# Optimization experiments

Hardware: AMD Instinct MI355X
Metric: run time of the kernel (lower is better)

Reference implementation:

```python
import jax, jax.numpy as jnp
import numpy as np

HID = 2048        # hidden_size
STATE = 128       # ssm state size N
HEADS = 64
HEADDIM = 64
GROUPS = 1
K = 4             # conv kernel
INTER = 4096      # expand * hidden_size == HEADS * HEADDIM
CONV_DIM = INTER + 2 * GROUPS * STATE   # 4352
PROJ = INTER + CONV_DIM + HEADS         # 8512
EPS = 1e-5


def setup_inputs() -> dict:
    ks = jax.random.split(jax.random.key(0), 8)
    hidden_states = jax.random.normal(ks[0], (2, 2048, HID), dtype=jnp.float32)
    norm_weight = jnp.ones((HID,), jnp.float32)
    in_proj_w = jax.random.normal(ks[1], (PROJ, HID), jnp.float32) * 0.02
    conv_w = jax.random.normal(ks[2], (CONV_DIM, 1, K), jnp.float32) * 0.1
    conv_b = jax.random.normal(ks[3], (CONV_DIM,), jnp.float32) * 0.02
    dt_bias = jax.random.normal(ks[4], (HEADS,), jnp.float32) * 0.5
    A_log = jnp.log(jnp.arange(1, HEADS + 1, dtype=jnp.float32))
    D = jnp.ones((HEADS,), jnp.float32)
    gate_norm_weight = jnp.ones((INTER,), jnp.float32)
    out_proj_w = jax.random.normal(ks[5], (HID, INTER), jnp.float32) * 0.02
    return {"hidden_states": hidden_states, "norm_weight": norm_weight,
            "in_proj_w": in_proj_w, "conv_w": conv_w, "conv_b": conv_b,
            "dt_bias": dt_bias, "A_log": A_log, "D": D,
            "gate_norm_weight": gate_norm_weight, "out_proj_w": out_proj_w}


def _rmsnorm(x, w, eps):
    v = jnp.mean(jnp.square(x.astype(jnp.float32)), axis=-1, keepdims=True)
    return (x * jax.lax.rsqrt(v + eps)) * w


def _mamba2_block(hidden_states, norm_weight, in_proj_w, conv_w, conv_b,
                  dt_bias, A_log, D, gate_norm_weight, out_proj_w):
    b, s, _ = hidden_states.shape
    residual = hidden_states.astype(jnp.float32)  # residual_in_fp32
    x = _rmsnorm(hidden_states, norm_weight, EPS)

    proj = x @ in_proj_w.T                                  # [b,s,PROJ]
    gate, xBC, dt = jnp.split(proj, [INTER, INTER + CONV_DIM], axis=-1)

    # causal depthwise conv1d over channels, then SiLU
    xBC_t = jnp.swapaxes(xBC, 1, 2)                          # [b,C,s]
    conv = jax.lax.conv_general_dilated(
        xBC_t, conv_w, window_strides=(1,), padding=[(K - 1, 0)],
        dimension_numbers=("NCH", "OIH", "NCH"), feature_group_count=CONV_DIM)
    xBC = jax.nn.silu(jnp.swapaxes(conv + conv_b[None, :, None], 1, 2))

    xs, B, C = jnp.split(xBC, [INTER, INTER + GROUPS * STATE], axis=-1)
    hg = HEADS // GROUPS
    xs = xs.reshape(b, s, GROUPS, hg, HEADDIM)
    B = B.reshape(b, s, GROUPS, STATE)
    C = C.reshape(b, s, GROUPS, STATE)

    dt = jax.nn.softplus(dt + dt_bias).reshape(b, s, GROUPS, hg)  # [b,s,g,hg]
    A = -jnp.exp(A_log).reshape(GROUPS, hg)
    dA = jnp.exp(dt * A)                                     # [b,s,g,hg]
    dtx = dt[..., None] * xs                                  # [b,s,g,hg,p]

    def step(state, inp):
        dA_t, dtx_t, B_t, C_t = inp
        # state: [b,g,hg,p,n]
        state = state * dA_t[..., None, None] + jnp.einsum("bghp,bgn->bghpn", dtx_t, B_t)
        y_t = jnp.einsum("bghpn,bgn->bghp", state, C_t)
        return state, y_t

    mv = lambda a: jnp.moveaxis(a, 1, 0)  # time-major for scan
    state0 = jnp.zeros((b, GROUPS, hg, HEADDIM, STATE), jnp.float32)
    _, y = jax.lax.scan(step, state0, (mv(dA), mv(dtx), mv(B), mv(C)))
    y = jnp.moveaxis(y, 0, 1)                                 # [b,s,g,hg,p]
    y = y + D.reshape(GROUPS, hg)[..., None] * xs             # skip term
    y = y.reshape(b, s, INTER)

    # gated RMSNorm then output projection
    y = _rmsnorm(y * jax.nn.silu(gate), gate_norm_weight, EPS)
    out = y @ out_proj_w.T
    return residual + out


def reference(hidden_states, norm_weight, in_proj_w, conv_w, conv_b,
              dt_bias, A_log, D, gate_norm_weight, out_proj_w):
    return _mamba2_block(hidden_states, norm_weight, in_proj_w, conv_w, conv_b,
                         dt_bias, A_log, D, gate_norm_weight, out_proj_w)
```

## Files before the change

### kernel.cpp

```cpp
#include <hip/hip_runtime.h>
#include <math.h>

#define HID      2048
#define STATE    128
#define HEADS    64
#define HEADDIM  64
#define INTER    4096
#define CONV_DIM 4352
#define PROJ     8512
#define NBATCH   2
#define SEQ      2048
#define BS       (NBATCH*SEQ)
#define EPS      1e-5f
#define YN_COL   4160

typedef __attribute__((ext_vector_type(8))) short short8;
typedef __attribute__((ext_vector_type(4))) float f32x4;

__device__ inline unsigned short f2bf(float f) {
  union { float f; unsigned int u; } v; v.f = f;
  unsigned int r = v.u + 0x7fffu + ((v.u >> 16) & 1u);
  return (unsigned short)(r >> 16);
}
__device__ inline float bf2f(unsigned short b) {
  union { unsigned int u; float f; } v; v.u = ((unsigned int)b) << 16;
  return v.f;
}

__global__ __launch_bounds__(256)
void cast_bf16_kernel(const float4* __restrict__ src, ushort4* __restrict__ dst, int n4) {
  int i = blockIdx.x * 256 + threadIdx.x;
  if (i >= n4) return;
  float4 v = src[i];
  ushort4 o;
  o.x = f2bf(v.x); o.y = f2bf(v.y); o.z = f2bf(v.z); o.w = f2bf(v.w);
  dst[i] = o;
}

__global__ __launch_bounds__(256)
void rmsnorm_in_kernel(const float* __restrict__ x, const float* __restrict__ w,
                       unsigned short* __restrict__ xn) {
  int row = blockIdx.x;
  int t = threadIdx.x;
  const float* xr = x + (size_t)row * HID;
  float4 a = ((const float4*)xr)[t];
  float4 b = ((const float4*)xr)[t + 256];
  float ss = a.x*a.x + a.y*a.y + a.z*a.z + a.w*a.w
           + b.x*b.x + b.y*b.y + b.z*b.z + b.w*b.w;
  for (int o = 32; o > 0; o >>= 1) ss += __shfl_down(ss, o);
  __shared__ float red[4];
  __shared__ float scl;
  if ((t & 63) == 0) red[t >> 6] = ss;
  __syncthreads();
  if (t == 0) scl = rsqrtf((red[0]+red[1]+red[2]+red[3]) / (float)HID + EPS);
  __syncthreads();
  float s = scl;
  float4 w0 = ((const float4*)w)[t];
  float4 w1 = ((const float4*)w)[t + 256];
  ushort4 o0, o1;
  o0.x = f2bf(a.x*s*w0.x); o0.y = f2bf(a.y*s*w0.y); o0.z = f2bf(a.z*s*w0.z); o0.w = f2bf(a.w*s*w0.w);
  o1.x = f2bf(b.x*s*w1.x); o1.y = f2bf(b.y*s*w1.y); o1.z = f2bf(b.z*s*w1.z); o1.w = f2bf(b.w*s*w1.w);
  ushort4* dst = (ushort4*)(xn + (size_t)row * HID);
  dst[t] = o0;
  dst[t + 256] = o1;
}


__device__ __forceinline__ void stage_half64(const unsigned short* __restrict__ G, int ld,
                                             int row0, int rmax, int kt,
                                             unsigned short* lbase, int half, int t) {
  const int w = t >> 6;
#pragma unroll
  for (int it = 0; it < 2; ++it) {
    int id = it * 256 + t;
    int rl = id >> 3;
    int sl = id & 7;
    int grow = row0 + half * 64 + rl;
    if (grow > rmax) grow = rmax;
    const unsigned short* g = G + (size_t)grow * ld + kt * 64 + ((sl ^ (rl & 7)) << 3);
    unsigned short* l = lbase + half * (64 * 64) + (it * 256 + w * 64) * 8;
    __builtin_amdgcn_global_load_lds((const __attribute__((address_space(1))) void*)g,
                                     (__attribute__((address_space(3))) void*)l, 16, 0, 0);
  }
}

#define VMW4 asm volatile("s_waitcnt vmcnt(4)" ::: "memory")

#define PHASE(BUF, MH, NH, RA, RB, STG, VMW_)                                        \
  {                                                                                  \
    const unsigned short* bufA = lds + (BUF)*16384;                                  \
    const unsigned short* bufB = lds + (BUF)*16384 + 8192;                           \
    if (RA) {                                                                        \
      _Pragma("unroll")                                                              \
      for (int ml = 0; ml < 2; ++ml) {                                               \
        _Pragma("unroll")                                                            \
        for (int kk = 0; kk < 2; ++kk) {                                             \
          const int r = wr*64 + (MH)*32 + ml*16 + tq;                                \
          aR[ml][kk] = *(const short8*)(bufA + r*64 + (((kk<<2)|quad)^(r&7))*8);     \
        }                                                                            \
      }                                                                              \
    }                                                                                \
    if (RB) {                                                                        \
      _Pragma("unroll")                                                              \
      for (int nl = 0; nl < 2; ++nl) {                                               \
        _Pragma("unroll")                                                            \
        for (int kk = 0; kk < 2; ++kk) {                                             \
          const int r = wc*64 + (NH)*32 + nl*16 + tq;                                \
          bR[NH][nl][kk] = *(const short8*)(bufB + r*64 + (((kk<<2)|quad)^(r&7))*8); \
        }                                                                            \
      }                                                                              \
    }                                                                                \
    STG;                                                                             \
    __builtin_amdgcn_s_barrier();                                                    \
    asm volatile("s_waitcnt lgkmcnt(0)" ::: "memory");                               \
    __builtin_amdgcn_sched_barrier(0);                                               \
    __builtin_amdgcn_s_setprio(1);                                                   \
    _Pragma("unroll")                                                                \
    for (int ml = 0; ml < 2; ++ml) {                                                 \
      _Pragma("unroll")                                                              \
      for (int nl = 0; nl < 2; ++nl) {                                               \
        _Pragma("unroll")                                                            \
        for (int kk = 0; kk < 2; ++kk) {                                             \
          acc[(MH)*2+ml][(NH)*2+nl] = __builtin_amdgcn_mfma_f32_16x16x32_bf16(       \
              aR[ml][kk], bR[NH][nl][kk], acc[(MH)*2+ml][(NH)*2+nl], 0, 0, 0);       \
        }                                                                            \
      }                                                                              \
    }                                                                                \
    __builtin_amdgcn_s_setprio(0);                                                   \
    VMW_;                                                                            \
    __builtin_amdgcn_s_barrier();                                                    \
  }

__global__ __launch_bounds__(256, 2)
void gemm128_kernel(const unsigned short* __restrict__ A, int lda,
                    const unsigned short* __restrict__ B,
                    float* __restrict__ Cf, unsigned short* __restrict__ Cb, int ldc,
                    int M, int N, int Kd, const float* __restrict__ residual) {
  __shared__ unsigned short lds[32768];
  const int t = threadIdx.x;
  const int lane = t & 63;
  const int quad = lane >> 4;
  const int tq = lane & 15;
  const int w = t >> 6;
  const int wr = w >> 1;
  const int wc = w & 1;

  const int Mtiles = M >> 7;
  const int Ntiles = (N + 127) >> 7;
  const int nwg = (int)gridDim.x;
  const int cpx = nwg >> 3;
  const int bid = (int)blockIdx.x;
  const int sw = (bid & 7) * cpx + (bid >> 3);
  const int NBfull = Ntiles & ~7;
  int m0, n0;
  if (sw < Mtiles * NBfull) {
    int brick = sw >> 6;
    int inner = sw & 63;
    int bm = brick % (Mtiles >> 3);
    int bn = brick / (Mtiles >> 3);
    m0 = (bm * 8 + (inner & 7)) << 7;
    n0 = (bn * 8 + (inner >> 3)) << 7;
  } else {
    int r = sw - Mtiles * NBfull;
    m0 = (r % Mtiles) << 7;
    n0 = (NBfull + r / Mtiles) << 7;
  }

  f32x4 acc[4][4];
#pragma unroll
  for (int i = 0; i < 4; ++i)
#pragma unroll
    for (int j = 0; j < 4; ++j) acc[i][j] = (f32x4){0.f, 0.f, 0.f, 0.f};

  short8 aR[2][2];
  short8 bR[2][2][2];

  unsigned short* A0 = lds;
  unsigned short* B0 = lds + 8192;
  unsigned short* A1 = lds + 16384;
  unsigned short* B1 = lds + 24576;

  const int kIters = Kd >> 6;
  const int nIter  = kIters >> 1;

  stage_half64(A, lda, m0, M - 1, 0, A0, 0, t);
  stage_half64(A, lda, m0, M - 1, 0, A0, 1, t);
  stage_half64(B, Kd,  n0, N - 1, 0, B0, 0, t);
  stage_half64(B, Kd,  n0, N - 1, 0, B0, 1, t);
  stage_half64(B, Kd,  n0, N - 1, 1, B1, 0, t);
  stage_half64(B, Kd,  n0, N - 1, 1, B1, 1, t);
  VMW4;
  __builtin_amdgcn_s_barrier();

  for (int i = 0; i < nIter; ++i) {
    const int k1 = 2 * i + 1;
    int k2 = 2 * i + 2; if (k2 > kIters - 1) k2 = kIters - 1;
    int k3 = 2 * i + 3; if (k3 > kIters - 1) k3 = kIters - 1;
    PHASE(0, 0, 0, 1, 1, stage_half64(A, lda, m0, M - 1, k1, A1, 0, t), ((void)0))
    PHASE(0, 0, 1, 0, 1, stage_half64(A, lda, m0, M - 1, k1, A1, 1, t), ((void)0))
    PHASE(0, 1, 1, 1, 0, stage_half64(B, Kd,  n0, N - 1, k2, B0, 0, t), ((void)0))
    PHASE(0, 1, 0, 0, 0, stage_half64(B, Kd,  n0, N - 1, k2, B0, 1, t), VMW4)
    PHASE(1, 0, 0, 1, 1, stage_half64(A, lda, m0, M - 1, k2, A0, 0, t), ((void)0))
    PHASE(1, 0, 1, 0, 1, stage_half64(A, lda, m0, M - 1, k2, A0, 1, t), ((void)0))
    PHASE(1, 1, 1, 1, 0, stage_half64(B, Kd,  n0, N - 1, k3, B1, 0, t), ((void)0))
    PHASE(1, 1, 0, 0, 0, stage_half64(B, Kd,  n0, N - 1, k3, B1, 1, t), VMW4)
  }
  asm volatile("s_waitcnt vmcnt(0)" ::: "memory");

#pragma unroll
  for (int mf = 0; mf < 4; ++mf) {
    const int rowb = m0 + wr * 64 + mf * 16 + quad * 4;
#pragma unroll
    for (int nf = 0; nf < 4; ++nf) {
      const int col = n0 + wc * 64 + nf * 16 + tq;
      if (col < N) {
        if (Cb) {
#pragma unroll
          for (int r = 0; r < 4; ++r)
            Cb[(size_t)(rowb + r) * ldc + col] = f2bf(acc[mf][nf][r]);
        } else {
#pragma unroll
          for (int r = 0; r < 4; ++r) {
            size_t idx = (size_t)(rowb + r) * N + col;
            float v = acc[mf][nf][r];
            if (residual) v += residual[idx];
            Cf[idx] = v;
          }
        }
      }
    }
  }
}

#define CONV_BC 128
#define CONV_BS 64
#define CXS 136

__global__ __launch_bounds__(256)
void conv_dt_kernel(const unsigned short* __restrict__ proj, const float* __restrict__ cw,
                    const float* __restrict__ cb, const float* __restrict__ dtb,
                    const float* __restrict__ A_log,
                    unsigned short* __restrict__ convo, float2* __restrict__ dts) {
  const int NCB = CONV_DIM / CONV_BC;
  const int NCONVB = NCB * (BS / CONV_BS);
  int blk = blockIdx.x;
  int t = threadIdx.x;
  if (blk < NCONVB) {
    __shared__ unsigned short xs[67 * CXS];
    int cblk = blk % NCB;
    int rblk = blk / NCB;
    int ch0 = cblk * CONV_BC;
    int rs0 = rblk * CONV_BS;
    int s0 = rs0 & (SEQ - 1);
    const int c8 = t & 15;
    const int co = c8 * 8;
    float cwr[4][8], cbr[8];
#pragma unroll
    for (int e = 0; e < 8; e++) {
      cbr[e] = cb[ch0 + co + e];
#pragma unroll
      for (int k = 0; k < 4; k++) cwr[k][e] = cw[(ch0 + co + e) * 4 + k];
    }
    for (int i = t; i < 67 * 16; i += 256) {
      int row = i >> 4, sl = i & 15;
      short8 v;
      if (s0 == 0 && row < 3) v = (short8){0,0,0,0,0,0,0,0};
      else v = *(const short8*)&proj[(size_t)(rs0 - 3 + row) * PROJ + INTER + ch0 + sl * 8];
      *(short8*)&xs[row * CXS + sl * 8] = v;
    }
    __syncthreads();
#pragma unroll
    for (int it = 0; it < 4; ++it) {
      int r = (t >> 4) + it * 16;
      float acc[8];
#pragma unroll
      for (int e = 0; e < 8; e++) acc[e] = cbr[e];
#pragma unroll
      for (int k = 0; k < 4; k++) {
        short8 v = *(const short8*)&xs[(r + k) * CXS + co];
#pragma unroll
        for (int e = 0; e < 8; e++) acc[e] += bf2f((unsigned short)v[e]) * cwr[k][e];
      }
      short8 o;
#pragma unroll
      for (int e = 0; e < 8; e++) {
        float a = acc[e];
        o[e] = (short)f2bf(a * __builtin_amdgcn_rcpf(1.f + __expf(-a)));
      }
      *(short8*)&convo[(size_t)(rs0 + r) * CONV_DIM + ch0 + co] = o;
    }
  } else {
    int k = (blk - NCONVB) * 256 + t;
    if (k < BS * HEADS) {
      int h  = k & 63;
      int rs = k >> 6;
      float x = bf2f(proj[(size_t)rs * PROJ + INTER + CONV_DIM + h]) + dtb[h];
      float dt = (x > 20.f) ? x : log1pf(__expf(x));
      float Ah = -__expf(A_log[h]);
      dts[k] = make_float2(dt, dt * Ah);
    }
  }
}

#define LCH 64
#define SR  128
#define BR  64
#define TST 72
#define SWZ(r,c) ((((c) ^ ((r) & 7)) << 3))
#define LBAR do { asm volatile("s_waitcnt lgkmcnt(0)" ::: "memory"); \
                  __builtin_amdgcn_s_barrier(); } while (0)

__global__ __launch_bounds__(512)
void ssd_scan_kernel(const unsigned short* __restrict__ convo, const float2* __restrict__ dts,
                     unsigned short* __restrict__ yp) {
  __shared__ unsigned short Cst[64 * SR];
  __shared__ unsigned short Bst[64 * SR];
  __shared__ unsigned short Btt[128 * BR];
  __shared__ unsigned short xtT[32 * TST];
  __shared__ unsigned short Msh[64 * TST];
  __shared__ unsigned short Sb[2][32 * SR];
  __shared__ float dtaL[64], dtvL[64];

  const int ph = blockIdx.x & 1;
  const int h  = (blockIdx.x >> 1) & 63;
  const int b  = blockIdx.x >> 7;
  const int t  = threadIdx.x;
  const int wv = t >> 6;
  const int lane = t & 63;
  const int quad = lane >> 4;
  const int tq   = lane & 15;
  const size_t row0 = (size_t)b * SEQ;
  const int xcol = h * 64 + ph * 32;

  for (int i = t; i < 32 * SR; i += 512) Sb[0][i] = 0;

  f32x4 s_acc[4];
#pragma unroll
  for (int c = 0; c < 4; c++) s_acc[c] = (f32x4){0.f, 0.f, 0.f, 0.f};
  const int pt  = wv & 1;
  const int ntb = ((wv >> 1) & 1) * 4;

  short8 vb_r[2], vc_r[2]; ushort4 vx_r; float2 dv_r = make_float2(0.f, 0.f);
  {
#pragma unroll
    for (int it = 0; it < 2; ++it) {
      int id = t + 512 * it;
      int row = id >> 4, cc = id & 15;
      size_t g = (row0 + row) * CONV_DIM + INTER;
      vb_r[it] = *(const short8*)&convo[g + cc * 8];
      vc_r[it] = *(const short8*)&convo[g + STATE + cc * 8];
    }
    int row = t >> 3, c = t & 7;
    vx_r = *(const ushort4*)&convo[(row0 + row) * CONV_DIM + xcol + c * 4];
    if (t < 64) dv_r = dts[((row0 + t) << 6) + h];
  }

  int pp = 0;
  for (int c0 = 0; c0 < SEQ; c0 += LCH, pp ^= 1) {
    LBAR;
#pragma unroll
    for (int it = 0; it < 2; ++it) {
      int id = t + 512 * it;
      int row = id >> 4, cc = id & 15;
      *(short8*)&Bst[row * SR + SWZ(row, cc)] = vb_r[it];
      *(short8*)&Cst[row * SR + SWZ(row, cc)] = vc_r[it];
    }
    {
      int row = t >> 3, c = t & 7;
      xtT[(c * 4 + 0) * TST + row] = vx_r.x;
      xtT[(c * 4 + 1) * TST + row] = vx_r.y;
      xtT[(c * 4 + 2) * TST + row] = vx_r.z;
      xtT[(c * 4 + 3) * TST + row] = vx_r.w;
    }
    if (t < 64) { dtvL[t] = dv_r.x; dtaL[t] = dv_r.y; }
    LBAR;

#pragma unroll
    for (int bi = 0; bi < 2; ++bi) {
      int q = t + 512 * bi;
      int n = q & 127, jc = q >> 7;
      short8 o;
#pragma unroll
      for (int s = 0; s < 8; ++s)
        o[s] = (short)Bst[(jc * 8 + s) * SR + SWZ(jc * 8 + s, n >> 3) + (n & 7)];
      *(short8*)&Btt[n * BR + SWZ(n, jc)] = o;
    }

    float v = dtaL[lane];
#pragma unroll
    for (int off = 1; off < 64; off <<= 1) {
      float u = __shfl_up(v, off);
      if (lane >= off) v += u;
    }
    float tot = __shfl(v, 63);

    LBAR;

    if (c0 + LCH < SEQ) {
#pragma unroll
      for (int it = 0; it < 2; ++it) {
        int id = t + 512 * it;
        int row = id >> 4, cc = id & 15;
        size_t g = (row0 + c0 + LCH + row) * CONV_DIM + INTER;
        vb_r[it] = *(const short8*)&convo[g + cc * 8];
        vc_r[it] = *(const short8*)&convo[g + STATE + cc * 8];
      }
      int row = t >> 3, c = t & 7;
      vx_r = *(const ushort4*)&convo[(row0 + c0 + LCH + row) * CONV_DIM + xcol + c * 4];
      if (t < 64) dv_r = dts[((row0 + c0 + LCH + t) << 6) + h];
    }

    if (wv < 4) {
      short8 afC[4];
#pragma unroll
      for (int kt = 0; kt < 4; kt++)
        afC[kt] = *(const short8*)&Cst[(16 * wv + tq) * SR + SWZ(16 * wv + tq, kt * 4 + quad)];
      f32x4 g_acc[4];
#pragma unroll
      for (int nj = 0; nj < 4; nj++) g_acc[nj] = (f32x4){0.f, 0.f, 0.f, 0.f};
#pragma unroll
      for (int kt = 0; kt < 4; kt++) {
#pragma unroll
        for (int nj = 0; nj < 4; nj++) {
          short8 bfr = *(const short8*)&Bst[(16 * nj + tq) * SR + SWZ(16 * nj + tq, kt * 4 + quad)];
          g_acc[nj] = __builtin_amdgcn_mfma_f32_16x16x32_bf16(afC[kt], bfr, g_acc[nj], 0, 0, 0);
        }
      }
      float ci[4], pex[4];
#pragma unroll
      for (int r = 0; r < 4; r++) {
        ci[r] = __shfl(v, 16 * wv + quad * 4 + r);
        pex[r] = __expf(ci[r]);
      }
#pragma unroll
      for (int nj = 0; nj < 4; nj++) {
        int j = 16 * nj + tq;
        float cj = __shfl(v, j);
        float dj = dtvL[j];
#pragma unroll
        for (int r = 0; r < 4; r++) {
          int i = 16 * wv + quad * 4 + r;
          float val = (j <= i) ? g_acc[nj][r] * __expf(ci[r] - cj) * dj : 0.f;
          Msh[i * TST + j] = f2bf(val);
        }
      }
      f32x4 yac[2];
      yac[0] = (f32x4){0.f, 0.f, 0.f, 0.f};
      yac[1] = (f32x4){0.f, 0.f, 0.f, 0.f};
#pragma unroll
      for (int kt = 0; kt < 4; kt++) {
#pragma unroll
        for (int np = 0; np < 2; np++) {
          short8 bs = *(const short8*)&Sb[pp][(16 * np + tq) * SR + SWZ(16 * np + tq, kt * 4 + quad)];
          yac[np] = __builtin_amdgcn_mfma_f32_16x16x32_bf16(afC[kt], bs, yac[np], 0, 0, 0);
        }
      }
#pragma unroll
      for (int np = 0; np < 2; np++)
#pragma unroll
        for (int r = 0; r < 4; r++) yac[np][r] *= pex[r];
#pragma unroll
      for (int kt2 = 0; kt2 < 2; kt2++) {
        short8 am = *(const short8*)&Msh[(16 * wv + tq) * TST + kt2 * 32 + quad * 8];
#pragma unroll
        for (int np = 0; np < 2; np++) {
          short8 bx = *(const short8*)&xtT[(16 * np + tq) * TST + kt2 * 32 + quad * 8];
          yac[np] = __builtin_amdgcn_mfma_f32_16x16x32_bf16(am, bx, yac[np], 0, 0, 0);
        }
      }
#pragma unroll
      for (int np = 0; np < 2; np++) {
#pragma unroll
        for (int r = 0; r < 4; r++) {
          int i = 16 * wv + quad * 4 + r;
          int p = ph * 32 + 16 * np + tq;
          yp[(row0 + c0 + i) * INTER + h * 64 + p] = f2bf(yac[np][r]);
        }
      }
    } else {
      float ptot = __expf(tot);
      short8 ax[2];
#pragma unroll
      for (int kt2 = 0; kt2 < 2; kt2++) {
        short8 xv = *(const short8*)&xtT[(16 * pt + tq) * TST + kt2 * 32 + quad * 8];
#pragma unroll
        for (int e = 0; e < 8; e++) {
          int j = kt2 * 32 + quad * 8 + e;
          float cj = __shfl(v, j);
          float wj = __expf(tot - cj) * dtvL[j];
          ax[kt2][e] = (short)f2bf(bf2f((unsigned short)xv[e]) * wj);
        }
      }
#pragma unroll
      for (int c = 0; c < 4; c++)
#pragma unroll
        for (int r = 0; r < 4; r++) s_acc[c][r] *= ptot;
#pragma unroll
      for (int kt2 = 0; kt2 < 2; kt2++) {
#pragma unroll
        for (int c = 0; c < 4; c++) {
          short8 bb = *(const short8*)&Btt[(16 * (ntb + c) + tq) * BR + SWZ(16 * (ntb + c) + tq, kt2 * 4 + quad)];
          s_acc[c] = __builtin_amdgcn_mfma_f32_16x16x32_bf16(ax[kt2], bb, s_acc[c], 0, 0, 0);
        }
      }
#pragma unroll
      for (int c = 0; c < 4; c++)
#pragma unroll
        for (int r = 0; r < 4; r++) {
          int p = 16 * pt + quad * 4 + r;
          int n = 16 * (ntb + c) + tq;
          Sb[pp ^ 1][p * SR + SWZ(p, n >> 3) + (n & 7)] = f2bf(s_acc[c][r]);
        }
    }
  }
}

__global__ __launch_bounds__(256)
void gated_norm_kernel(const unsigned short* __restrict__ yp,
                       const unsigned short* __restrict__ convo, const unsigned short* __restrict__ proj,
                       const float* __restrict__ Dv, const float* __restrict__ gnw,
                       unsigned short* __restrict__ yn) {
  int row = blockIdx.x;
  int t = threadIdx.x;
  __shared__ float red[4];
  __shared__ float scl;
  size_t yo = (size_t)row * INTER;
  size_t co = (size_t)row * CONV_DIM;
  size_t po = (size_t)row * PROJ;
  float vv[16];
  float ss = 0.f;
#pragma unroll
  for (int c = 0; c < 4; c++) {
    int i = t * 4 + c * 1024;
    ushort4 y0 = *(const ushort4*)&yp[yo + i];
    ushort4 xs = *(const ushort4*)&convo[co + i];
    ushort4 g  = *(const ushort4*)&proj[po + i];
    float Dh = Dv[i >> 6];
    float yv[4] = { bf2f(y0.x) + Dh * bf2f(xs.x),
                    bf2f(y0.y) + Dh * bf2f(xs.y),
                    bf2f(y0.z) + Dh * bf2f(xs.z),
                    bf2f(y0.w) + Dh * bf2f(xs.w) };
    float gv[4] = { bf2f(g.x), bf2f(g.y), bf2f(g.z), bf2f(g.w) };
#pragma unroll
    for (int k = 0; k < 4; k++) {
      float val = yv[k] * (gv[k] * __builtin_amdgcn_rcpf(1.f + __expf(-gv[k])));
      vv[c * 4 + k] = val;
      ss += val * val;
    }
  }
  for (int o = 32; o > 0; o >>= 1) ss += __shfl_down(ss, o);
  if ((t & 63) == 0) red[t >> 6] = ss;
  __syncthreads();
  if (t == 0) scl = rsqrtf((red[0]+red[1]+red[2]+red[3]) / (float)INTER + EPS);
  __syncthreads();
  float s = scl;
#pragma unroll
  for (int c = 0; c < 4; c++) {
    int i = t * 4 + c * 1024;
    ushort4 o;
    o.x = f2bf(vv[c*4+0] * s * gnw[i + 0]);
    o.y = f2bf(vv[c*4+1] * s * gnw[i + 1]);
    o.z = f2bf(vv[c*4+2] * s * gnw[i + 2]);
    o.w = f2bf(vv[c*4+3] * s * gnw[i + 3]);
    *(ushort4*)&yn[po + i] = o;
  }
}

extern "C" void kernel_launch(void* const* d_in, const int* in_sizes, int n_in,
                              void* d_out, int out_size, void* d_ws, size_t ws_size,
                              hipStream_t stream) {
  const float* hidden  = (const float*)d_in[0];
  const float* norm_w  = (const float*)d_in[1];
  const float* w1      = (const float*)d_in[2];
  const float* convw   = (const float*)d_in[3];
  const float* convb   = (const float*)d_in[4];
  const float* dt_bias = (const float*)d_in[5];
  const float* A_log   = (const float*)d_in[6];
  const float* Dv      = (const float*)d_in[7];
  const float* gnw     = (const float*)d_in[8];
  const float* w2      = (const float*)d_in[9];
  float* out = (float*)d_out;

  char* ws = (char*)d_ws;
  size_t off = 0;
  auto alloc = [&](size_t bytes) {
    void* p = ws + off;
    off += (bytes + 255) & ~(size_t)255;
    return p;
  };
  unsigned short* XN  = (unsigned short*)alloc((size_t)BS * HID * 2);
  unsigned short* W1B = (unsigned short*)alloc((size_t)PROJ * HID * 2);
  unsigned short* W2B = (unsigned short*)alloc((size_t)HID * INTER * 2);
  unsigned short* PRJ = (unsigned short*)alloc((size_t)BS * PROJ * 2);
  unsigned short* CVO = (unsigned short*)alloc((size_t)BS * CONV_DIM * 2);
  float2*         DTS = (float2*)alloc((size_t)BS * HEADS * 8);
  unsigned short* YP  = XN;
  unsigned short* YN  = PRJ + YN_COL;
  if (off > ws_size) return;
  (void)in_sizes; (void)n_in; (void)out_size;

  int n1 = PROJ * HID / 4;
  cast_bf16_kernel<<<(n1 + 255) / 256, 256, 0, stream>>>((const float4*)w1, (ushort4*)W1B, n1);
  int n2 = HID * INTER / 4;
  cast_bf16_kernel<<<(n2 + 255) / 256, 256, 0, stream>>>((const float4*)w2, (ushort4*)W2B, n2);

  rmsnorm_in_kernel<<<BS, 256, 0, stream>>>(hidden, norm_w, XN);

  gemm128_kernel<<<dim3((BS / 128) * ((PROJ + 127) / 128)), 256, 0, stream>>>(
      XN, HID, W1B, nullptr, PRJ, PROJ, BS, PROJ, HID, nullptr);

  conv_dt_kernel<<<(CONV_DIM / CONV_BC) * (BS / CONV_BS) + (BS * HEADS) / 256, 256, 0, stream>>>(
      PRJ, convw, convb, dt_bias, A_log, CVO, DTS);

  ssd_scan_kernel<<<256, 512, 0, stream>>>(CVO, DTS, YP);

  gated_norm_kernel<<<BS, 256, 0, stream>>>(YP, CVO, PRJ, Dv, gnw, YN);

  gemm128_kernel<<<dim3((BS / 128) * (HID / 128)), 256, 0, stream>>>(
      YN, PROJ, W2B, out, nullptr, HID, BS, HID, INTER, hidden);
}
```

Before: 528.8 us.

## Make GEMM kernels persistent with atomic tile counter scheduling

Both GEMMs now launch a fixed grid of 512 workgroups that pull tiles from a global atomic counter until all tiles are done, instead of one workgroup per tile with a swizzled brick mapping. This aims to cut tail imbalance and launch overhead. The trade-off is a simple column-major tile order (m fastest) in place of the L2-friendly 8x8 brick swizzle, plus one atomic and extra barriers per tile. A memset resets the counters on every call.

```diff
diff --git a/kernel.cpp b/kernel.cpp
--- a/kernel.cpp
+++ b/kernel.cpp
@@ -135,8 +135,10 @@
 void gemm128_kernel(const unsigned short* __restrict__ A, int lda,
                     const unsigned short* __restrict__ B,
                     float* __restrict__ Cf, unsigned short* __restrict__ Cb, int ldc,
-                    int M, int N, int Kd, const float* __restrict__ residual) {
+                    int M, int N, int Kd, const float* __restrict__ residual,
+                    unsigned int* __restrict__ counter, int nTiles) {
   __shared__ unsigned short lds[32768];
+  __shared__ unsigned int sw_sh;
   const int t = threadIdx.x;
   const int lane = t & 63;
   const int quad = lane >> 4;
@@ -146,89 +148,79 @@
   const int wc = w & 1;
 
   const int Mtiles = M >> 7;
-  const int Ntiles = (N + 127) >> 7;
-  const int nwg = (int)gridDim.x;
-  const int cpx = nwg >> 3;
-  const int bid = (int)blockIdx.x;
-  const int sw = (bid & 7) * cpx + (bid >> 3);
-  const int NBfull = Ntiles & ~7;
-  int m0, n0;
-  if (sw < Mtiles * NBfull) {
-    int brick = sw >> 6;
-    int inner = sw & 63;
-    int bm = brick % (Mtiles >> 3);
-    int bn = brick / (Mtiles >> 3);
-    m0 = (bm * 8 + (inner & 7)) << 7;
-    n0 = (bn * 8 + (inner >> 3)) << 7;
-  } else {
-    int r = sw - Mtiles * NBfull;
-    m0 = (r % Mtiles) << 7;
-    n0 = (NBfull + r / Mtiles) << 7;
-  }
-
-  f32x4 acc[4][4];
-#pragma unroll
-  for (int i = 0; i < 4; ++i)
-#pragma unroll
-    for (int j = 0; j < 4; ++j) acc[i][j] = (f32x4){0.f, 0.f, 0.f, 0.f};
-
-  short8 aR[2][2];
-  short8 bR[2][2][2];
+  const int kIters = Kd >> 6;
+  const int nIter  = kIters >> 1;
 
   unsigned short* A0 = lds;
   unsigned short* B0 = lds + 8192;
   unsigned short* A1 = lds + 16384;
   unsigned short* B1 = lds + 24576;
 
-  const int kIters = Kd >> 6;
-  const int nIter  = kIters >> 1;
-
-  stage_half64(A, lda, m0, M - 1, 0, A0, 0, t);
-  stage_half64(A, lda, m0, M - 1, 0, A0, 1, t);
-  stage_half64(B, Kd,  n0, N - 1, 0, B0, 0, t);
-  stage_half64(B, Kd,  n0, N - 1, 0, B0, 1, t);
-  stage_half64(B, Kd,  n0, N - 1, 1, B1, 0, t);
-  stage_half64(B, Kd,  n0, N - 1, 1, B1, 1, t);
-  VMW4;
-  __builtin_amdgcn_s_barrier();
-
-  for (int i = 0; i < nIter; ++i) {
-    const int k1 = 2 * i + 1;
-    int k2 = 2 * i + 2; if (k2 > kIters - 1) k2 = kIters - 1;
-    int k3 = 2 * i + 3; if (k3 > kIters - 1) k3 = kIters - 1;
-    PHASE(0, 0, 0, 1, 1, stage_half64(A, lda, m0, M - 1, k1, A1, 0, t), ((void)0))
-    PHASE(0, 0, 1, 0, 1, stage_half64(A, lda, m0, M - 1, k1, A1, 1, t), ((void)0))
-    PHASE(0, 1, 1, 1, 0, stage_half64(B, Kd,  n0, N - 1, k2, B0, 0, t), ((void)0))
-    PHASE(0, 1, 0, 0, 0, stage_half64(B, Kd,  n0, N - 1, k2, B0, 1, t), VMW4)
-    PHASE(1, 0, 0, 1, 1, stage_half64(A, lda, m0, M - 1, k2, A0, 0, t), ((void)0))
-    PHASE(1, 0, 1, 0, 1, stage_half64(A, lda, m0, M - 1, k2, A0, 1, t), ((void)0))
-    PHASE(1, 1, 1, 1, 0, stage_half64(B, Kd,  n0, N - 1, k3, B1, 0, t), ((void)0))
-    PHASE(1, 1, 0, 0, 0, stage_half64(B, Kd,  n0, N - 1, k3, B1, 1, t), VMW4)
-  }
-  asm volatile("s_waitcnt vmcnt(0)" ::: "memory");
-
-#pragma unroll
-  for (int mf = 0; mf < 4; ++mf) {
-    const int rowb = m0 + wr * 64 + mf * 16 + quad * 4;
-#pragma unroll
-    for (int nf = 0; nf < 4; ++nf) {
-      const int col = n0 + wc * 64 + nf * 16 + tq;
-      if (col < N) {
-        if (Cb) {
-#pragma unroll
-          for (int r = 0; r < 4; ++r)
-            Cb[(size_t)(rowb + r) * ldc + col] = f2bf(acc[mf][nf][r]);
-        } else {
-#pragma unroll
-          for (int r = 0; r < 4; ++r) {
-            size_t idx = (size_t)(rowb + r) * N + col;
-            float v = acc[mf][nf][r];
-            if (residual) v += residual[idx];
-            Cf[idx] = v;
+  short8 aR[2][2];
+  short8 bR[2][2][2];
+
+  for (;;) {
+    if (t == 0) sw_sh = atomicAdd(counter, 1u);
+    __syncthreads();
+    const unsigned int sw = sw_sh;
+    if (sw >= (unsigned int)nTiles) break;
+    const int m0 = (int)(sw % (unsigned int)Mtiles) << 7;
+    const int n0 = (int)(sw / (unsigned int)Mtiles) << 7;
+
+    f32x4 acc[4][4];
+#pragma unroll
+    for (int i = 0; i < 4; ++i)
+#pragma unroll
+      for (int j = 0; j < 4; ++j) acc[i][j] = (f32x4){0.f, 0.f, 0.f, 0.f};
+
+    stage_half64(A, lda, m0, M - 1, 0, A0, 0, t);
+    stage_half64(A, lda, m0, M - 1, 0, A0, 1, t);
+    stage_half64(B, Kd,  n0, N - 1, 0, B0, 0, t);
+    stage_half64(B, Kd,  n0, N - 1, 0, B0, 1, t);
+    stage_half64(B, Kd,  n0, N - 1, 1, B1, 0, t);
+    stage_half64(B, Kd,  n0, N - 1, 1, B1, 1, t);
+    VMW4;
+    __builtin_amdgcn_s_barrier();
+
+    for (int i = 0; i < nIter; ++i) {
+      const int k1 = 2 * i + 1;
+      int k2 = 2 * i + 2; if (k2 > kIters - 1) k2 = kIters - 1;
+      int k3 = 2 * i + 3; if (k3 > kIters - 1) k3 = kIters - 1;
+      PHASE(0, 0, 0, 1, 1, stage_half64(A, lda, m0, M - 1, k1, A1, 0, t), ((void)0))
+      PHASE(0, 0, 1, 0, 1, stage_half64(A, lda, m0, M - 1, k1, A1, 1, t), ((void)0))
+      PHASE(0, 1, 1, 1, 0, stage_half64(B, Kd,  n0, N - 1, k2, B0, 0, t), ((void)0))
+      PHASE(0, 1, 0, 0, 0, stage_half64(B, Kd,  n0, N - 1, k2, B0, 1, t), VMW4)
+      PHASE(1, 0, 0, 1, 1, stage_half64(A, lda, m0, M - 1, k2, A0, 0, t), ((void)0))
+      PHASE(1, 0, 1, 0, 1, stage_half64(A, lda, m0, M - 1, k2, A0, 1, t), ((void)0))
+      PHASE(1, 1, 1, 1, 0, stage_half64(B, Kd,  n0, N - 1, k3, B1, 0, t), ((void)0))
+      PHASE(1, 1, 0, 0, 0, stage_half64(B, Kd,  n0, N - 1, k3, B1, 1, t), VMW4)
+    }
+    asm volatile("s_waitcnt vmcnt(0)" ::: "memory");
+
+#pragma unroll
+    for (int mf = 0; mf < 4; ++mf) {
+      const int rowb = m0 + wr * 64 + mf * 16 + quad * 4;
+#pragma unroll
+      for (int nf = 0; nf < 4; ++nf) {
+        const int col = n0 + wc * 64 + nf * 16 + tq;
+        if (col < N) {
+          if (Cb) {
+#pragma unroll
+            for (int r = 0; r < 4; ++r)
+              Cb[(size_t)(rowb + r) * ldc + col] = f2bf(acc[mf][nf][r]);
+          } else {
+#pragma unroll
+            for (int r = 0; r < 4; ++r) {
+              size_t idx = (size_t)(rowb + r) * N + col;
+              float v = acc[mf][nf][r];
+              if (residual) v += residual[idx];
+              Cf[idx] = v;
+            }
           }
         }
       }
     }
+    __syncthreads();
   }
 }
 
@@ -588,6 +580,7 @@
     off += (bytes + 255) & ~(size_t)255;
     return p;
   };
+  unsigned int*   CTR = (unsigned int*)alloc(256);
   unsigned short* XN  = (unsigned short*)alloc((size_t)BS * HID * 2);
   unsigned short* W1B = (unsigned short*)alloc((size_t)PROJ * HID * 2);
   unsigned short* W2B = (unsigned short*)alloc((size_t)HID * INTER * 2);
@@ -599,6 +592,8 @@
   if (off > ws_size) return;
   (void)in_sizes; (void)n_in; (void)out_size;
 
+  hipMemsetAsync(CTR, 0, 256, stream);
+
   int n1 = PROJ * HID / 4;
   cast_bf16_kernel<<<(n1 + 255) / 256, 256, 0, stream>>>((const float4*)w1, (ushort4*)W1B, n1);
   int n2 = HID * INTER / 4;
@@ -606,8 +601,9 @@
 
   rmsnorm_in_kernel<<<BS, 256, 0, stream>>>(hidden, norm_w, XN);
 
-  gemm128_kernel<<<dim3((BS / 128) * ((PROJ + 127) / 128)), 256, 0, stream>>>(
-      XN, HID, W1B, nullptr, PRJ, PROJ, BS, PROJ, HID, nullptr);
+  gemm128_kernel<<<512, 256, 0, stream>>>(
+      XN, HID, W1B, nullptr, PRJ, PROJ, BS, PROJ, HID, nullptr,
+      CTR, (BS / 128) * ((PROJ + 127) / 128));
 
   conv_dt_kernel<<<(CONV_DIM / CONV_BC) * (BS / CONV_BS) + (BS * HEADS) / 256, 256, 0, stream>>>(
       PRJ, convw, convb, dt_bias, A_log, CVO, DTS);
@@ -616,6 +612,7 @@
 
   gated_norm_kernel<<<BS, 256, 0, stream>>>(YP, CVO, PRJ, Dv, gnw, YN);
 
-  gemm128_kernel<<<dim3((BS / 128) * (HID / 128)), 256, 0, stream>>>(
-      YN, PROJ, W2B, out, nullptr, HID, BS, HID, INTER, hidden);
-}
+  gemm128_kernel<<<512, 256, 0, stream>>>(
+      YN, PROJ, W2B, out, nullptr, HID, BS, HID, INTER, hidden,
+      CTR + 32, (BS / 128) * (HID / 128));
+}
```

Result: slower. 561.3 us (+6.1%).
